# Performance work log

Measured on AMD Instinct MI355X. Metric: run time of the kernel, lower is better.

The kernel has to match this reference:

```python
import jax, jax.numpy as jnp
import numpy as np

B, L, D, NH = 4, 1024, 1024, 16
DH = D // NH
H = 8 * D // 3  # SwiGLU hidden = 2730
NEG = -1e9


def setup_inputs() -> dict:
    key = jax.random.key(0)
    ks = jax.random.split(key, 8)
    init = lambda k, shape: (jax.random.normal(k, shape, jnp.float32) * 0.02)
    x = jax.random.normal(ks[0], (B, L, D), jnp.float32)
    causal = jnp.tril(jnp.ones((L, L), bool))
    m = jnp.where(causal, 0.0, NEG)[None, None].astype(jnp.float32)  # [1,1,L,L]
    return {
        'x': x,
        'm': m,
        'wx': init(ks[1], (D, 3 * D)),
        'bx': jnp.zeros((3 * D,), jnp.float32),
        'wo': init(ks[2], (D, D)),
        'bo': jnp.zeros((D,), jnp.float32),
        'mhanorm_w': jnp.ones((D,), jnp.float32),
        'ffnorm_w': jnp.ones((D,), jnp.float32),
        'u': init(ks[3], (D, H)),
        'v': init(ks[4], (D, H)),
        'w': init(ks[5], (H, D)),
    }


def rmsnorm(x, weight, eps=1e-8):
    rrms = jax.lax.rsqrt(jnp.mean(x * x, axis=-1, keepdims=True) + eps)
    return weight * x * rrms


def reference(x, m, wx, bx, wo, bo, mhanorm_w, ffnorm_w, u, v, w):
    scale = D ** (-0.5)  # note: original uses d**-0.5, NOT dh**-0.5
    qkv = rmsnorm(x, mhanorm_w) @ wx + bx                 # [B,L,3D]
    q, k, vv = jnp.split(qkv, 3, axis=-1)                  # each [B,L,D]
    split = lambda t: t.reshape(B, L, NH, DH).transpose(0, 2, 1, 3)  # [B,NH,L,DH]
    q, k, vv = split(q), split(k), split(vv)               # pe = identity (default)
    scores = jnp.einsum('bhic,bhjc->bhij', q, k) * scale + m
    A = jax.nn.softmax(scores, axis=-1)
    head = jnp.einsum('bhij,bhjc->bhic', A, vv)            # [B,NH,L,DH]
    head = head.transpose(0, 2, 1, 3).reshape(B, L, D)
    x = x + head @ wo + bo
    xn = rmsnorm(x, ffnorm_w)
    return x + (jax.nn.silu(xn @ u) * (xn @ v)) @ w
```

## Files before the change

### kernel.cpp

```cpp
#include <hip/hip_runtime.h>

#define B_  4
#define L_  1024
#define D_  1024
#define NH_ 16
#define DH_ 64
#define H_  2730
#define HP_ 2816
#define M_  4096

typedef short bf16x8 __attribute__((ext_vector_type(8)));
typedef float f32x4  __attribute__((ext_vector_type(4)));

__device__ __forceinline__ unsigned short f2bf(float f) {
    unsigned int u = __builtin_bit_cast(unsigned int, f);
    u += 0x7fffu + ((u >> 16) & 1u);
    return (unsigned short)(u >> 16);
}
__device__ __forceinline__ float bf2f(unsigned short s) {
    unsigned int u = ((unsigned int)s) << 16;
    return __builtin_bit_cast(float, u);
}

__device__ __forceinline__ void glds16(const void* g, void* l) {
    __builtin_amdgcn_global_load_lds(
        (const __attribute__((address_space(1))) unsigned int*)g,
        (__attribute__((address_space(3))) unsigned int*)l, 16, 0, 0);
}

__device__ __forceinline__ void xcd_swz(int& lx, int& ly) {
    const int gx = gridDim.x;
    const int cpx = gx >> 1;
    const int flat = blockIdx.x + gx * blockIdx.y;
    const int x = flat & 7, j = flat >> 3;
    ly = (x >> 1) * 8 + (j & 7);
    lx = (x & 1) * cpx + (j >> 3);
}

__global__ __launch_bounds__(256) void cvtT_rms_all(
    const float* __restrict__ wx, const float* __restrict__ wo,
    const float* __restrict__ u,  const float* __restrict__ v,
    const float* __restrict__ w,
    const float* __restrict__ x,  const float* __restrict__ mhw,
    unsigned short* __restrict__ wxb, unsigned short* __restrict__ wob,
    unsigned short* __restrict__ ub,  unsigned short* __restrict__ vb,
    unsigned short* __restrict__ wb,  unsigned short* __restrict__ xnb)
{
    __shared__ float t[32][33];
    __shared__ float red[4];
    const int id = blockIdx.x;

    if (id >= 12544) {
        const int row = id - 12544;
        const int tt = threadIdx.x;
        const float4 vv = ((const float4*)(x + (size_t)row * 1024))[tt];
        float ss = vv.x*vv.x + vv.y*vv.y + vv.z*vv.z + vv.w*vv.w;
        #pragma unroll
        for (int off = 32; off > 0; off >>= 1) ss += __shfl_down(ss, off);
        if ((tt & 63) == 0) red[tt >> 6] = ss;
        __syncthreads();
        const float tot = red[0] + red[1] + red[2] + red[3];
        const float rr = rsqrtf(tot * (1.0f / 1024.0f) + 1e-8f);
        const float4 wv = ((const float4*)mhw)[tt];
        ushort4 o;
        o.x = f2bf(vv.x * wv.x * rr); o.y = f2bf(vv.y * wv.y * rr);
        o.z = f2bf(vv.z * wv.z * rr); o.w = f2bf(vv.w * wv.w * rr);
        ((ushort4*)(xnb + (size_t)row * 1024))[tt] = o;
        return;
    }

    const float* in; unsigned short* out;
    int K, N, Kp, gx, base;
    if (id < 3072)      { in = wx; out = wxb; K = 1024; N = 3072; Kp = 1024; gx = 32; base = 0; }
    else if (id < 4096) { in = wo; out = wob; K = 1024; N = 1024; Kp = 1024; gx = 32; base = 3072; }
    else if (id < 6912) { in = u;  out = ub;  K = 1024; N = 2730; Kp = 1024; gx = 32; base = 4096; }
    else if (id < 9728) { in = v;  out = vb;  K = 1024; N = 2730; Kp = 1024; gx = 32; base = 6912; }
    else                { in = w;  out = wb;  K = 2730; N = 1024; Kp = 2816; gx = 88; base = 9728; }
    const int local = id - base;
    const int bx = local % gx, by = local / gx;

    const int k0 = bx * 32, n0 = by * 32;
    const int tx = threadIdx.x & 31, ty = threadIdx.x >> 5;
    #pragma unroll
    for (int i = 0; i < 4; ++i) {
        const int k = k0 + ty + i * 8, n = n0 + tx;
        t[ty + i * 8][tx] = (k < K && n < N) ? in[(size_t)k * N + n] : 0.0f;
    }
    __syncthreads();
    #pragma unroll
    for (int i = 0; i < 4; ++i) {
        const int n = n0 + ty + i * 8, k = k0 + tx;
        out[(size_t)n * Kp + k] = f2bf(t[tx][ty + i * 8]);
    }
}

__global__ __launch_bounds__(256) void rmsnorm_kernel(
    const float* __restrict__ x, const float* __restrict__ w,
    unsigned short* __restrict__ out)
{
    const int row = blockIdx.x;
    const int t = threadIdx.x;
    const float4 v = ((const float4*)(x + (size_t)row * 1024))[t];
    float ss = v.x*v.x + v.y*v.y + v.z*v.z + v.w*v.w;
    #pragma unroll
    for (int off = 32; off > 0; off >>= 1) ss += __shfl_down(ss, off);
    __shared__ float red[4];
    if ((t & 63) == 0) red[t >> 6] = ss;
    __syncthreads();
    const float tot = red[0] + red[1] + red[2] + red[3];
    const float rr = rsqrtf(tot * (1.0f / 1024.0f) + 1e-8f);
    const float4 wv = ((const float4*)w)[t];
    ushort4 o;
    o.x = f2bf(v.x * wv.x * rr); o.y = f2bf(v.y * wv.y * rr);
    o.z = f2bf(v.z * wv.z * rr); o.w = f2bf(v.w * wv.w * rr);
    ((ushort4*)(out + (size_t)row * 1024))[t] = o;
}

template<int EPI, int TN>
__global__ __launch_bounds__(256) void gemm_bf16(
    const unsigned short* __restrict__ A, const unsigned short* __restrict__ Bt,
    int M, int N, int K,
    const float* __restrict__ bias, const float* __restrict__ res,
    float* __restrict__ outf, unsigned short* __restrict__ outb)
{
    constexpr int NS = TN / 32;
    constexpr int G  = (TN == 128) ? 4 : 3;
    constexpr int WAIT_G = 0xF70 | G;
    __shared__ __align__(16) unsigned short As[2][128 * 32];
    __shared__ __align__(16) unsigned short Bs[2][TN * 32];
    const int tid = threadIdx.x;
    int lx, ly;
    xcd_swz(lx, ly);
    const int m0 = ly * 128, n0 = lx * TN;
    const int lane = tid & 63, w = tid >> 6;
    const int wm = w >> 1, wn = w & 1;
    const int quad = lane >> 4, l15 = lane & 15;

    f32x4 acc[4][NS] = {};

    const int p0 = w * 64 + lane;
    const int r0 = p0 >> 2, c0 = (p0 & 3) ^ ((r0 >> 1) & 3);
    const int offL0 = p0 * 8, offL1 = 2048 + p0 * 8;

    const unsigned short* Ag0 = A + (size_t)(m0 + r0) * K + c0 * 8;
    const unsigned short* Ag1 = A + (size_t)(m0 + 64 + r0) * K + c0 * 8;
    const unsigned short* Bg0 = Bt + (size_t)(n0 + r0) * K + c0 * 8;
    const unsigned short* Bg1 = Bt + (size_t)(n0 + 64 + r0) * K + c0 * 8;

    auto stage = [&](int kk, int buf) {
        glds16(Ag0 + kk, &As[buf][offL0]);
        glds16(Ag1 + kk, &As[buf][offL1]);
        glds16(Bg0 + kk, &Bs[buf][offL0]);
        if (TN == 128) glds16(Bg1 + kk, &Bs[buf][offL1]);
    };
    auto compute = [&](int buf) {
        bf16x8 af[4], bfr[NS];
        #pragma unroll
        for (int ms = 0; ms < 4; ++ms) {
            const int row = wm * 64 + ms * 16 + l15;
            af[ms] = *(const bf16x8*)&As[buf][row * 32 + ((quad ^ ((row >> 1) & 3)) * 8)];
        }
        #pragma unroll
        for (int ns = 0; ns < NS; ++ns) {
            const int row = wn * (TN / 2) + ns * 16 + l15;
            bfr[ns] = *(const bf16x8*)&Bs[buf][row * 32 + ((quad ^ ((row >> 1) & 3)) * 8)];
        }
        #pragma unroll
        for (int ms = 0; ms < 4; ++ms)
            #pragma unroll
            for (int ns = 0; ns < NS; ++ns)
                acc[ms][ns] = __builtin_amdgcn_mfma_f32_16x16x32_bf16(
                    af[ms], bfr[ns], acc[ms][ns], 0, 0, 0);
    };

    const int nk = K >> 5;
    stage(0, 0);
    for (int i = 0; i < nk; i += 2) {
        if (i + 1 < nk) { stage((i + 1) << 5, 1); __builtin_amdgcn_s_waitcnt(WAIT_G); }
        else            { __builtin_amdgcn_s_waitcnt(0xF70); }
        __builtin_amdgcn_s_barrier();
        compute(0);
        __builtin_amdgcn_s_barrier();
        if (i + 2 < nk) { stage((i + 2) << 5, 0); __builtin_amdgcn_s_waitcnt(WAIT_G); }
        else            { __builtin_amdgcn_s_waitcnt(0xF70); }
        __builtin_amdgcn_s_barrier();
        compute(1);
        __builtin_amdgcn_s_barrier();
    }

    #pragma unroll
    for (int ms = 0; ms < 4; ++ms) {
        #pragma unroll
        for (int r = 0; r < 4; ++r) {
            const int row = m0 + wm * 64 + ms * 16 + quad * 4 + r;
            const size_t ro = (size_t)row * N;
            #pragma unroll
            for (int ns = 0; ns < NS; ++ns) {
                const int col = n0 + wn * (TN / 2) + ns * 16 + l15;
                float v = acc[ms][ns][r];
                if (EPI == 0) {
                    outb[ro + col] = f2bf(v + bias[col]);
                } else if (EPI == 1) {
                    outf[ro + col] = v + bias[col] + res[ro + col];
                } else {
                    outf[ro + col] = v + res[ro + col];
                }
            }
        }
    }
}

template<int EPI>
__global__ __launch_bounds__(256) void gemm_k64(
    const unsigned short* __restrict__ A, const unsigned short* __restrict__ Bt,
    int M, int N, int K,
    const float* __restrict__ bias, const float* __restrict__ res,
    float* __restrict__ outf, unsigned short* __restrict__ outb)
{
    __shared__ __align__(16) unsigned short As[2][128 * 64];
    __shared__ __align__(16) unsigned short Bs[2][64 * 64];
    const int tid = threadIdx.x;
    int lx, ly;
    xcd_swz(lx, ly);
    const int m0 = ly * 128, n0 = lx * 64;
    const int lane = tid & 63, w = tid >> 6;
    const int wm = w >> 1, wn = w & 1;
    const int quad = lane >> 4, l15 = lane & 15;

    f32x4 acc[4][2] = {};

    const unsigned short* Ag[4];
    const unsigned short* Bg[2];
    int offA[4], offB[2];
    #pragma unroll
    for (int i = 0; i < 4; ++i) {
        const int p = tid + i * 256, r = p >> 3, c = (p & 7) ^ (r & 7);
        Ag[i] = A + (size_t)(m0 + r) * K + c * 8;
        offA[i] = p * 8;
    }
    #pragma unroll
    for (int i = 0; i < 2; ++i) {
        const int p = tid + i * 256, r = p >> 3, c = (p & 7) ^ (r & 7);
        Bg[i] = Bt + (size_t)(n0 + r) * K + c * 8;
        offB[i] = p * 8;
    }

    auto stage = [&](int kk, int buf) {
        #pragma unroll
        for (int i = 0; i < 4; ++i) glds16(Ag[i] + kk, &As[buf][offA[i]]);
        #pragma unroll
        for (int i = 0; i < 2; ++i) glds16(Bg[i] + kk, &Bs[buf][offB[i]]);
    };
    auto compute = [&](int buf) {
        bf16x8 af[4][2], bfr[2][2];
        #pragma unroll
        for (int ms = 0; ms < 4; ++ms) {
            const int row = wm * 64 + ms * 16 + l15;
            #pragma unroll
            for (int kk = 0; kk < 2; ++kk)
                af[ms][kk] = *(const bf16x8*)&As[buf][row * 64 + (((kk * 4 + quad) ^ (row & 7)) * 8)];
        }
        #pragma unroll
        for (int ns = 0; ns < 2; ++ns) {
            const int row = wn * 32 + ns * 16 + l15;
            #pragma unroll
            for (int kk = 0; kk < 2; ++kk)
                bfr[ns][kk] = *(const bf16x8*)&Bs[buf][row * 64 + (((kk * 4 + quad) ^ (row & 7)) * 8)];
        }
        #pragma unroll
        for (int kk = 0; kk < 2; ++kk)
            #pragma unroll
            for (int ms = 0; ms < 4; ++ms)
                #pragma unroll
                for (int ns = 0; ns < 2; ++ns)
                    acc[ms][ns] = __builtin_amdgcn_mfma_f32_16x16x32_bf16(
                        af[ms][kk], bfr[ns][kk], acc[ms][ns], 0, 0, 0);
    };

    const int nk = K >> 6;
    stage(0, 0);
    for (int i = 0; i < nk; i += 2) {
        if (i + 1 < nk) { stage((i + 1) << 6, 1); __builtin_amdgcn_s_waitcnt(0xF76); }
        else            { __builtin_amdgcn_s_waitcnt(0xF70); }
        __builtin_amdgcn_s_barrier();
        compute(0);
        __builtin_amdgcn_s_barrier();
        if (i + 2 < nk) { stage((i + 2) << 6, 0); __builtin_amdgcn_s_waitcnt(0xF76); }
        else            { __builtin_amdgcn_s_waitcnt(0xF70); }
        __builtin_amdgcn_s_barrier();
        compute(1);
        __builtin_amdgcn_s_barrier();
    }

    #pragma unroll
    for (int ms = 0; ms < 4; ++ms) {
        #pragma unroll
        for (int r = 0; r < 4; ++r) {
            const int row = m0 + wm * 64 + ms * 16 + quad * 4 + r;
            const size_t ro = (size_t)row * N;
            #pragma unroll
            for (int ns = 0; ns < 2; ++ns) {
                const int col = n0 + wn * 32 + ns * 16 + l15;
                float v = acc[ms][ns][r];
                if (EPI == 0) {
                    outb[ro + col] = f2bf(v + bias[col]);
                } else if (EPI == 1) {
                    outf[ro + col] = v + bias[col] + res[ro + col];
                } else {
                    outf[ro + col] = v + res[ro + col];
                }
            }
        }
    }
}

__global__ __launch_bounds__(256, 2) void gemm_swiglu(
    const unsigned short* __restrict__ A, const unsigned short* __restrict__ Bu,
    const unsigned short* __restrict__ Bv, unsigned short* __restrict__ g)
{
    constexpr int K = 1024, N = HP_;
    constexpr int WAIT_G = 0xF76;
    __shared__ __align__(16) unsigned short As[2][128 * 32];
    __shared__ __align__(16) unsigned short Us[2][128 * 32];
    __shared__ __align__(16) unsigned short Vs[2][128 * 32];
    const int tid = threadIdx.x;
    int lx, ly;
    xcd_swz(lx, ly);
    const int m0 = ly * 128, n0 = lx * 128;
    const int lane = tid & 63, w = tid >> 6;
    const int wm = w >> 1, wn = w & 1;
    const int quad = lane >> 4, l15 = lane & 15;

    f32x4 au[4][4] = {}, av[4][4] = {};

    const int p0 = w * 64 + lane;
    const int r0 = p0 >> 2, c0 = (p0 & 3) ^ ((r0 >> 1) & 3);
    const int offL0 = p0 * 8, offL1 = 2048 + p0 * 8;

    const unsigned short* Ag0 = A  + (size_t)(m0 + r0) * K + c0 * 8;
    const unsigned short* Ag1 = A  + (size_t)(m0 + 64 + r0) * K + c0 * 8;
    const unsigned short* Ug0 = Bu + (size_t)(n0 + r0) * K + c0 * 8;
    const unsigned short* Ug1 = Bu + (size_t)(n0 + 64 + r0) * K + c0 * 8;
    const unsigned short* Vg0 = Bv + (size_t)(n0 + r0) * K + c0 * 8;
    const unsigned short* Vg1 = Bv + (size_t)(n0 + 64 + r0) * K + c0 * 8;

    auto stage = [&](int kk, int buf) {
        glds16(Ag0 + kk, &As[buf][offL0]);
        glds16(Ag1 + kk, &As[buf][offL1]);
        glds16(Ug0 + kk, &Us[buf][offL0]);
        glds16(Ug1 + kk, &Us[buf][offL1]);
        glds16(Vg0 + kk, &Vs[buf][offL0]);
        glds16(Vg1 + kk, &Vs[buf][offL1]);
    };
    auto compute = [&](int buf) {
        bf16x8 af[4], uf[4], vf[4];
        #pragma unroll
        for (int ms = 0; ms < 4; ++ms) {
            const int row = wm * 64 + ms * 16 + l15;
            af[ms] = *(const bf16x8*)&As[buf][row * 32 + ((quad ^ ((row >> 1) & 3)) * 8)];
        }
        #pragma unroll
        for (int ns = 0; ns < 4; ++ns) {
            const int row = wn * 64 + ns * 16 + l15;
            uf[ns] = *(const bf16x8*)&Us[buf][row * 32 + ((quad ^ ((row >> 1) & 3)) * 8)];
            vf[ns] = *(const bf16x8*)&Vs[buf][row * 32 + ((quad ^ ((row >> 1) & 3)) * 8)];
        }
        #pragma unroll
        for (int ms = 0; ms < 4; ++ms)
            #pragma unroll
            for (int ns = 0; ns < 4; ++ns) {
                au[ms][ns] = __builtin_amdgcn_mfma_f32_16x16x32_bf16(af[ms], uf[ns], au[ms][ns], 0, 0, 0);
                av[ms][ns] = __builtin_amdgcn_mfma_f32_16x16x32_bf16(af[ms], vf[ns], av[ms][ns], 0, 0, 0);
            }
    };

    stage(0, 0);
    for (int i = 0; i < 32; i += 2) {
        if (i + 1 < 32) { stage((i + 1) << 5, 1); __builtin_amdgcn_s_waitcnt(WAIT_G); }
        else            { __builtin_amdgcn_s_waitcnt(0xF70); }
        __builtin_amdgcn_s_barrier();
        compute(0);
        __builtin_amdgcn_s_barrier();
        if (i + 2 < 32) { stage((i + 2) << 5, 0); __builtin_amdgcn_s_waitcnt(WAIT_G); }
        else            { __builtin_amdgcn_s_waitcnt(0xF70); }
        __builtin_amdgcn_s_barrier();
        compute(1);
        __builtin_amdgcn_s_barrier();
    }

    #pragma unroll
    for (int ms = 0; ms < 4; ++ms) {
        #pragma unroll
        for (int r = 0; r < 4; ++r) {
            const int row = m0 + wm * 64 + ms * 16 + quad * 4 + r;
            const size_t ro = (size_t)row * N;
            #pragma unroll
            for (int ns = 0; ns < 4; ++ns) {
                const int col = n0 + wn * 64 + ns * 16 + l15;
                const float uu = au[ms][ns][r];
                const float vv = av[ms][ns][r];
                g[ro + col] = f2bf(uu / (1.0f + __expf(-uu)) * vv);
            }
        }
    }
}

__global__ __launch_bounds__(256) void attn_mfma2_kernel(
    const unsigned short* __restrict__ qkv, unsigned short* __restrict__ hout)
{
    __shared__ __align__(16) unsigned short Qs[64 * 72];
    __shared__ __align__(16) unsigned short Ks[2][64 * 64];
    __shared__ __align__(16) unsigned short Vt[2][64 * 72];
    __shared__ __align__(16) unsigned short Ps[64 * 68];

    const int tid = threadIdx.x;
    const int d = blockIdx.x + 8 * blockIdx.y + 128 * blockIdx.z;
    const int qa = d >> 6;
    const int hb = d & 63;
    const int h = hb & 15, b = hb >> 4;
    const int qb = 15 - qa;
    const int w = tid >> 6, lane = tid & 63;
    const int quad = lane >> 4, l15 = lane & 15;

    const size_t basek = (size_t)(b * L_) * 3072 + 1024 + h * 64;
    const size_t basev = basek + 1024;

    const int qr6 = tid >> 2, qq4 = tid & 3;
    auto stageQ = [&](int qtile) {
        const int grow = qtile * 64 + qr6;
        const unsigned short* gp = qkv + (size_t)(b * L_ + grow) * 3072 + h * 64 + qq4 * 16;
        uint4 a0 = *(const uint4*)gp;
        uint4 a1 = *(const uint4*)(gp + 8);
        unsigned short* dp = &Qs[qr6 * 72 + qq4 * 16];
        *(uint4*)dp = a0; *(uint4*)(dp + 8) = a1;
    };
    stageQ(qa);

    auto stageK = [&](int kt, int buf) {
        #pragma unroll
        for (int i = 0; i < 2; ++i) {
            const int p = i * 256 + tid;
            const int row = p >> 3;
            const int cc = (p & 7) ^ (row & 7);
            glds16(qkv + basek + (size_t)(kt * 64 + row) * 3072 + cc * 8, &Ks[buf][p * 8]);
        }
    };
    const int vkey = (tid & 31) * 2, vdp = tid >> 5;
    auto loadV = [&](int kt, uint4& v0, uint4& v1) {
        const unsigned short* gp = qkv + basev + (size_t)(kt * 64 + vkey) * 3072 + vdp * 8;
        v0 = *(const uint4*)gp;
        v1 = *(const uint4*)(gp + 3072);
    };
    auto writeV = [&](int buf, const uint4& v0, const uint4& v1) {
        union { uint4 u; unsigned short s[8]; } a, c;
        a.u = v0; c.u = v1;
        #pragma unroll
        for (int i = 0; i < 8; ++i) {
            unsigned int pk = (unsigned int)a.s[i] | ((unsigned int)c.s[i] << 16);
            *(unsigned int*)&Vt[buf][(vdp * 8 + i) * 72 + vkey] = pk;
        }
    };

    f32x4 O[4] = {};
    float l4[4] = {0.0f, 0.0f, 0.0f, 0.0f};

    stageK(0, 0);
    {
        uint4 v0, v1;
        loadV(0, v0, v1);
        writeV(0, v0, v1);
    }
    __syncthreads();

    bf16x8 af[2];
    #pragma unroll
    for (int s = 0; s < 2; ++s)
        af[s] = *(const bf16x8*)&Qs[(w * 16 + l15) * 72 + s * 32 + quad * 8];

    const float SCL2 = 0.045084220027779984f;

    int qsel = 0, kt = 0;
    for (int t = 0; t < 17; ++t) {
        if (t == qa + 1) {
            #pragma unroll
            for (int s = 0; s < 2; ++s)
                af[s] = *(const bf16x8*)&Qs[(w * 16 + l15) * 72 + s * 32 + quad * 8];
        }
        const int cb = t & 1, nb = cb ^ 1;
        const bool havenext = (t < 16);
        uint4 nv0, nv1;
        if (havenext) {
            const int ktn = (t + 1 <= qa) ? (t + 1) : (t - qa);
            stageK(ktn, nb);
            loadV(ktn, nv0, nv1);
        }

        bf16x8 bfk[4][2];
        #pragma unroll
        for (int n = 0; n < 4; ++n) {
            const int row = n * 16 + l15;
            #pragma unroll
            for (int s = 0; s < 2; ++s)
                bfk[n][s] = *(const bf16x8*)&Ks[cb][row * 64 + (((s * 4 + quad) ^ (row & 7)) * 8)];
        }
        f32x4 sacc[4] = {};
        __builtin_amdgcn_s_setprio(1);
        #pragma unroll
        for (int n = 0; n < 4; ++n) {
            sacc[n] = __builtin_amdgcn_mfma_f32_16x16x32_bf16(af[0], bfk[n][0], sacc[n], 0, 0, 0);
            sacc[n] = __builtin_amdgcn_mfma_f32_16x16x32_bf16(af[1], bfk[n][1], sacc[n], 0, 0, 0);
        }
        __builtin_amdgcn_s_setprio(0);

        const bool diag = (kt == (qsel ? qb : qa));
        float rs[4] = {0.0f, 0.0f, 0.0f, 0.0f};
        #pragma unroll
        for (int n = 0; n < 4; ++n) {
            const int col = n * 16 + l15;
            #pragma unroll
            for (int r = 0; r < 4; ++r) {
                float e = __builtin_amdgcn_exp2f(sacc[n][r] * SCL2);
                if (diag && col > (w * 16 + quad * 4 + r)) e = 0.0f;
                Ps[(w * 16 + quad * 4 + r) * 68 + col] = f2bf(e);
                rs[r] += e;
            }
        }

        if (havenext) writeV(nb, nv0, nv1);

        bf16x8 ap[2], bv[4][2];
        #pragma unroll
        for (int s = 0; s < 2; ++s)
            ap[s] = *(const bf16x8*)&Ps[(w * 16 + l15) * 68 + s * 32 + quad * 8];
        #pragma unroll
        for (int dn = 0; dn < 4; ++dn)
            #pragma unroll
            for (int s = 0; s < 2; ++s)
                bv[dn][s] = *(const bf16x8*)&Vt[cb][(dn * 16 + l15) * 72 + s * 32 + quad * 8];
        __builtin_amdgcn_s_setprio(1);
        #pragma unroll
        for (int dn = 0; dn < 4; ++dn) {
            O[dn] = __builtin_amdgcn_mfma_f32_16x16x32_bf16(ap[0], bv[dn][0], O[dn], 0, 0, 0);
            O[dn] = __builtin_amdgcn_mfma_f32_16x16x32_bf16(ap[1], bv[dn][1], O[dn], 0, 0, 0);
        }
        __builtin_amdgcn_s_setprio(0);

        #pragma unroll
        for (int r = 0; r < 4; ++r) {
            #pragma unroll
            for (int m = 1; m < 16; m <<= 1)
                rs[r] += __shfl_xor(rs[r], m);
            l4[r] += rs[r];
        }

        if (t == qa) {
            #pragma unroll
            for (int r = 0; r < 4; ++r) {
                const float inv = 1.0f / l4[r];
                const int grow = qa * 64 + w * 16 + quad * 4 + r;
                unsigned short* op = hout + (size_t)(b * L_ + grow) * 1024 + h * 64;
                #pragma unroll
                for (int dn = 0; dn < 4; ++dn)
                    op[dn * 16 + l15] = f2bf(O[dn][r] * inv);
            }
            #pragma unroll
            for (int dn = 0; dn < 4; ++dn)
                #pragma unroll
                for (int r = 0; r < 4; ++r) O[dn][r] = 0.0f;
            #pragma unroll
            for (int r = 0; r < 4; ++r) l4[r] = 0.0f;
            qsel = 1;
            kt = 0;
            stageQ(qb);
        } else {
            ++kt;
        }
        __syncthreads();
    }

    #pragma unroll
    for (int r = 0; r < 4; ++r) {
        const float inv = 1.0f / l4[r];
        const int grow = qb * 64 + w * 16 + quad * 4 + r;
        unsigned short* op = hout + (size_t)(b * L_ + grow) * 1024 + h * 64;
        #pragma unroll
        for (int dn = 0; dn < 4; ++dn)
            op[dn * 16 + l15] = f2bf(O[dn][r] * inv);
    }
}

extern "C" void kernel_launch(void* const* d_in, const int* in_sizes, int n_in,
                              void* d_out, int out_size, void* d_ws, size_t ws_size,
                              hipStream_t stream)
{
    const float* x   = (const float*)d_in[0];
    const float* wx  = (const float*)d_in[2];
    const float* bx  = (const float*)d_in[3];
    const float* wo  = (const float*)d_in[4];
    const float* bo  = (const float*)d_in[5];
    const float* mhw = (const float*)d_in[6];
    const float* ffw = (const float*)d_in[7];
    const float* u   = (const float*)d_in[8];
    const float* v   = (const float*)d_in[9];
    const float* w   = (const float*)d_in[10];
    float* out = (float*)d_out;

    char* W = (char*)d_ws;
    unsigned short* xn_bf   = (unsigned short*)(W + 0);
    unsigned short* wx_bf   = (unsigned short*)(W + 8388608);
    unsigned short* qkv_bf  = (unsigned short*)(W + 14680064);
    unsigned short* head_bf = (unsigned short*)(W + 39845888);
    unsigned short* wo_bf   = (unsigned short*)(W + 48234496);
    float*          x2      = (float*)(W + 50331648);
    unsigned short* u_bf    = (unsigned short*)(W + 67108864);
    unsigned short* v_bf    = (unsigned short*)(W + 72876032);
    unsigned short* w_bf    = (unsigned short*)(W + 78643200);
    unsigned short* g_bf    = (unsigned short*)(W + 84410368);

    cvtT_rms_all<<<16640, 256, 0, stream>>>(wx, wo, u, v, w, x, mhw,
                                            wx_bf, wo_bf, u_bf, v_bf, w_bf, xn_bf);

    gemm_bf16<0, 128><<<dim3(3072 / 128, 32), 256, 0, stream>>>(
        xn_bf, wx_bf, 4096, 3072, 1024, bx, nullptr, nullptr, qkv_bf);

    attn_mfma2_kernel<<<dim3(8, 16, 4), 256, 0, stream>>>(qkv_bf, head_bf);

    gemm_k64<1><<<dim3(1024 / 64, 32), 256, 0, stream>>>(
        head_bf, wo_bf, 4096, 1024, 1024, bo, x, x2, nullptr);

    rmsnorm_kernel<<<4096, 256, 0, stream>>>(x2, ffw, xn_bf);

    gemm_swiglu<<<dim3(2816 / 128, 32), 256, 0, stream>>>(xn_bf, u_bf, v_bf, g_bf);

    gemm_k64<4><<<dim3(1024 / 64, 32), 256, 0, stream>>>(
        g_bf, w_bf, 4096, 1024, 2816, nullptr, x2, out, nullptr);
}
```

Measured before the change: 325.4 us.

## Widen QKV GEMM tile to 192 columns and load attention Q directly to registers

The QKV projection GEMM now uses 128x192 tiles, with staging loops generalised over the number of B chunks. This cuts the grid from 768 to 512 blocks and raises arithmetic intensity per block, at the cost of more accumulator registers and less parallelism. The attention kernel drops its shared-memory Q staging buffer and loads the Q MFMA fragments straight from global memory into registers. That removes an LDS round trip and frees shared memory.

```diff
diff --git a/kernel.cpp b/kernel.cpp
--- a/kernel.cpp
+++ b/kernel.cpp
@@ -123,8 +123,9 @@
     const float* __restrict__ bias, const float* __restrict__ res,
     float* __restrict__ outf, unsigned short* __restrict__ outb)
 {
-    constexpr int NS = TN / 32;
-    constexpr int G  = (TN == 128) ? 4 : 3;
+    constexpr int NS  = TN / 32;
+    constexpr int BCH = TN / 64;
+    constexpr int G   = 2 + BCH;
     constexpr int WAIT_G = 0xF70 | G;
     __shared__ __align__(16) unsigned short As[2][128 * 32];
     __shared__ __align__(16) unsigned short Bs[2][TN * 32];
@@ -138,20 +139,26 @@
 
     f32x4 acc[4][NS] = {};
 
-    const int p0 = w * 64 + lane;
-    const int r0 = p0 >> 2, c0 = (p0 & 3) ^ ((r0 >> 1) & 3);
-    const int offL0 = p0 * 8, offL1 = 2048 + p0 * 8;
-
-    const unsigned short* Ag0 = A + (size_t)(m0 + r0) * K + c0 * 8;
-    const unsigned short* Ag1 = A + (size_t)(m0 + 64 + r0) * K + c0 * 8;
-    const unsigned short* Bg0 = Bt + (size_t)(n0 + r0) * K + c0 * 8;
-    const unsigned short* Bg1 = Bt + (size_t)(n0 + 64 + r0) * K + c0 * 8;
+    const unsigned short* Ag[2]; int offA[2];
+    const unsigned short* Bg[BCH]; int offB[BCH];
+    #pragma unroll
+    for (int i = 0; i < 2; ++i) {
+        const int p = tid + i * 256, r = p >> 2, c = (p & 3) ^ ((r >> 1) & 3);
+        Ag[i] = A + (size_t)(m0 + r) * K + c * 8;
+        offA[i] = p * 8;
+    }
+    #pragma unroll
+    for (int i = 0; i < BCH; ++i) {
+        const int p = tid + i * 256, r = p >> 2, c = (p & 3) ^ ((r >> 1) & 3);
+        Bg[i] = Bt + (size_t)(n0 + r) * K + c * 8;
+        offB[i] = p * 8;
+    }
 
     auto stage = [&](int kk, int buf) {
-        glds16(Ag0 + kk, &As[buf][offL0]);
-        glds16(Ag1 + kk, &As[buf][offL1]);
-        glds16(Bg0 + kk, &Bs[buf][offL0]);
-        if (TN == 128) glds16(Bg1 + kk, &Bs[buf][offL1]);
+        #pragma unroll
+        for (int i = 0; i < 2; ++i) glds16(Ag[i] + kk, &As[buf][offA[i]]);
+        #pragma unroll
+        for (int i = 0; i < BCH; ++i) glds16(Bg[i] + kk, &Bs[buf][offB[i]]);
     };
     auto compute = [&](int buf) {
         bf16x8 af[4], bfr[NS];
@@ -408,7 +415,6 @@
 __global__ __launch_bounds__(256) void attn_mfma2_kernel(
     const unsigned short* __restrict__ qkv, unsigned short* __restrict__ hout)
 {
-    __shared__ __align__(16) unsigned short Qs[64 * 72];
     __shared__ __align__(16) unsigned short Ks[2][64 * 64];
     __shared__ __align__(16) unsigned short Vt[2][64 * 72];
     __shared__ __align__(16) unsigned short Ps[64 * 68];
@@ -425,16 +431,14 @@
     const size_t basek = (size_t)(b * L_) * 3072 + 1024 + h * 64;
     const size_t basev = basek + 1024;
 
-    const int qr6 = tid >> 2, qq4 = tid & 3;
-    auto stageQ = [&](int qtile) {
-        const int grow = qtile * 64 + qr6;
-        const unsigned short* gp = qkv + (size_t)(b * L_ + grow) * 3072 + h * 64 + qq4 * 16;
-        uint4 a0 = *(const uint4*)gp;
-        uint4 a1 = *(const uint4*)(gp + 8);
-        unsigned short* dp = &Qs[qr6 * 72 + qq4 * 16];
-        *(uint4*)dp = a0; *(uint4*)(dp + 8) = a1;
-    };
-    stageQ(qa);
+    bf16x8 af[2];
+    auto loadQ = [&](int qtile) {
+        const unsigned short* gp = qkv +
+            (size_t)(b * L_ + qtile * 64 + w * 16 + l15) * 3072 + h * 64 + quad * 8;
+        af[0] = *(const bf16x8*)gp;
+        af[1] = *(const bf16x8*)(gp + 32);
+    };
+    loadQ(qa);
 
     auto stageK = [&](int kt, int buf) {
         #pragma unroll
@@ -472,20 +476,10 @@
     }
     __syncthreads();
 
-    bf16x8 af[2];
-    #pragma unroll
-    for (int s = 0; s < 2; ++s)
-        af[s] = *(const bf16x8*)&Qs[(w * 16 + l15) * 72 + s * 32 + quad * 8];
-
     const float SCL2 = 0.045084220027779984f;
 
     int qsel = 0, kt = 0;
     for (int t = 0; t < 17; ++t) {
-        if (t == qa + 1) {
-            #pragma unroll
-            for (int s = 0; s < 2; ++s)
-                af[s] = *(const bf16x8*)&Qs[(w * 16 + l15) * 72 + s * 32 + quad * 8];
-        }
         const int cb = t & 1, nb = cb ^ 1;
         const bool havenext = (t < 16);
         uint4 nv0, nv1;
@@ -571,7 +565,7 @@
             for (int r = 0; r < 4; ++r) l4[r] = 0.0f;
             qsel = 1;
             kt = 0;
-            stageQ(qb);
+            loadQ(qb);
         } else {
             ++kt;
         }
@@ -620,7 +614,7 @@
     cvtT_rms_all<<<16640, 256, 0, stream>>>(wx, wo, u, v, w, x, mhw,
                                             wx_bf, wo_bf, u_bf, v_bf, w_bf, xn_bf);
 
-    gemm_bf16<0, 128><<<dim3(3072 / 128, 32), 256, 0, stream>>>(
+    gemm_bf16<0, 192><<<dim3(3072 / 192, 32), 256, 0, stream>>>(
         xn_bf, wx_bf, 4096, 3072, 1024, bx, nullptr, nullptr, qkv_bf);
 
     attn_mfma2_kernel<<<dim3(8, 16, 4), 256, 0, stream>>>(qkv_bf, head_bf);
```

New measurement: 355.4 us. 1.09x slower.
